# Performance work log

Measured on AMD Instinct MI355X. Metric: run time of the kernel, lower is better.

## Reference

```python
import jax, jax.numpy as jnp
import numpy as np
import math

THETA = 10000.0

def apply_rope(x):
    # x: [B, H, S, D] with D even; interleaved even/odd rotation
    B, H, S, D = x.shape
    dim_half = D // 2
    freq_idx = jnp.arange(dim_half, dtype=jnp.float32)
    inv_freq = jnp.exp(-math.log(THETA) * freq_idx * 2.0 / D)  # [D/2]
    pos = jnp.arange(S, dtype=jnp.float32)
    angles = pos[:, None] * inv_freq[None, :]      # [S, D/2]
    cos = jnp.cos(angles)[None, None]              # [1,1,S,D/2]
    sin = jnp.sin(angles)[None, None]
    x_even = x[..., ::2]
    x_odd = x[..., 1::2]
    r_even = x_even * cos - x_odd * sin
    r_odd = x_odd * cos + x_even * sin
    return jnp.stack([r_even, r_odd], axis=-1).reshape(B, H, S, D)

def setup_inputs() -> dict:
    key = jax.random.key(0)
    ks = jax.random.split(key, 5)
    B, S, E = 2, 2048, 1024
    std = 0.02
    inp = {
        "hidden_states": jax.random.normal(ks[0], (B, S, E), dtype=jnp.float32),
        "Wq": jax.random.normal(ks[1], (E, E), dtype=jnp.float32) * std,
        "bq": jnp.zeros((E,), dtype=jnp.float32),
        "Wk": jax.random.normal(ks[2], (E, E), dtype=jnp.float32) * std,
        "bk": jnp.zeros((E,), dtype=jnp.float32),
        "Wv": jax.random.normal(ks[3], (E, E), dtype=jnp.float32) * std,
        "bv": jnp.zeros((E,), dtype=jnp.float32),
        "Wo": jax.random.normal(ks[4], (E, E), dtype=jnp.float32) * std,
        "bo": jnp.zeros((E,), dtype=jnp.float32),
    }
    return inp

def reference(hidden_states, Wq, bq, Wk, bk, Wv, bv, Wo, bo):
    NUM_HEADS = 16
    B, S, E = hidden_states.shape
    D = E // NUM_HEADS
    scale = 1.0 / math.sqrt(D)

    def proj(W, b):
        # torch Linear: x @ W.T + b; then [B,S,H,D] -> [B,H,S,D]
        y = hidden_states @ W.T + b
        return y.reshape(B, S, NUM_HEADS, D).transpose(0, 2, 1, 3)

    q = apply_rope(proj(Wq, bq))
    k = apply_rope(proj(Wk, bk))
    v = proj(Wv, bv)

    scores = jnp.einsum("bhqd,bhkd->bhqk", q, k) * scale
    attn = jax.nn.softmax(scores, axis=-1)
    out = jnp.einsum("bhqk,bhkd->bhqd", attn, v)  # [B,H,S,D]
    out = out.transpose(0, 2, 1, 3).reshape(B, S, E)
    return out @ Wo.T + bo  # dropout: eval mode (identity)
```

## Files before the change

kernel.cpp:

```cpp
#include <hip/hip_runtime.h>
#include <math.h>

#define B_ 2
#define S_ 2048
#define E_ 1024
#define H_ 16
#define D_ 64
#define M_ (B_*S_)
#define PT 32

typedef short bf16x8 __attribute__((ext_vector_type(8)));
typedef float f32x4 __attribute__((ext_vector_type(4)));
typedef unsigned short u16x4 __attribute__((ext_vector_type(4)));

__device__ __forceinline__ unsigned short f2bf(float f) {
    unsigned int u = __builtin_bit_cast(unsigned int, f);
    u += 0x7FFFu + ((u >> 16) & 1u);
    return (unsigned short)(u >> 16);
}
__device__ __forceinline__ f32x4 mfma16(bf16x8 a, bf16x8 b, f32x4 c) {
    return __builtin_amdgcn_mfma_f32_16x16x32_bf16(a, b, c, 0, 0, 0);
}
__device__ __forceinline__ bf16x8 cvt8(const float* p) {
    f32x4 lo = *(const f32x4*)p;
    f32x4 hi = *(const f32x4*)(p + 4);
    bf16x8 r;
#pragma unroll
    for (int e = 0; e < 4; e++) { r[e] = (short)f2bf(lo[e]); r[e + 4] = (short)f2bf(hi[e]); }
    return r;
}
__device__ __forceinline__ void g2l16(const unsigned short* g, unsigned short* l) {
    __builtin_amdgcn_global_load_lds(
        (const __attribute__((address_space(1))) unsigned int*)(const void*)g,
        (__attribute__((address_space(3))) unsigned int*)(void*)l,
        16, 0, 0);
}

__global__ __launch_bounds__(256) void cvt_kernel(
    const float* __restrict__ X,  const float* __restrict__ Wq,
    const float* __restrict__ Wk, const float* __restrict__ Wv,
    const float* __restrict__ Wo,
    unsigned short* __restrict__ Xb, unsigned short* __restrict__ Wb)
{
    const int y = blockIdx.y;
    const float* src = (y == 0) ? X : (y == 1) ? Wq : (y == 2) ? Wk : (y == 3) ? Wv : Wo;
    unsigned short* dst = (y == 0) ? Xb : Wb + (size_t)(y - 1) * (E_ * E_);
    const size_t n = (y == 0) ? (size_t)M_ * E_ : (size_t)E_ * E_;
    size_t i = ((size_t)blockIdx.x * 256 + threadIdx.x) * 8;
    if (i < n) *(bf16x8*)(dst + i) = cvt8(src + i);
}

__global__ __launch_bounds__(256, 4) void qkv_rope_bf(
    const unsigned short* __restrict__ Xb, const unsigned short* __restrict__ Wb,
    const float* __restrict__ bq, const float* __restrict__ bk,
    const float* __restrict__ bv,
    unsigned short* __restrict__ Qo, unsigned short* __restrict__ Ko,
    unsigned short* __restrict__ Vo)
{
    __shared__ __align__(16) unsigned char lds_raw[128 * 132 * 2];
    unsigned short* As = (unsigned short*)lds_raw;
    unsigned short* Bs = (unsigned short*)(lds_raw + 8192);
    unsigned short* Cs = (unsigned short*)lds_raw;

    const int t = threadIdx.x;
    const int w = t >> 6, lane = t & 63, quad = lane >> 4, l16 = lane & 15;
    const int wr = (w >> 1) * 64, wc = (w & 1) * 64;
    const int n0 = blockIdx.x * 128, m0 = blockIdx.y * 128;
    const int z = blockIdx.z;
    const unsigned short* W = Wb + (size_t)z * (E_ * E_);
    const float* bias = (z == 0) ? bq : (z == 1) ? bk : bv;

    const int r4 = t >> 2, c8 = (t & 3) * 8;
    const unsigned short* Ag = Xb + (size_t)(m0 + r4) * E_ + c8;
    const unsigned short* Bg = W  + (size_t)(n0 + r4) * E_ + c8;

    f32x4 zero = {0.f, 0.f, 0.f, 0.f};
    f32x4 acc[4][4];
#pragma unroll
    for (int i = 0; i < 4; i++)
#pragma unroll
        for (int j = 0; j < 4; j++) acc[i][j] = zero;

    for (int kt = 0; kt < E_; kt += 32) {
        __syncthreads();
        g2l16(Ag + kt,           &As[t * 8]);
        g2l16(Ag + 64 * E_ + kt, &As[t * 8 + 2048]);
        g2l16(Bg + kt,           &Bs[t * 8]);
        g2l16(Bg + 64 * E_ + kt, &Bs[t * 8 + 2048]);
        __syncthreads();
        bf16x8 af[4], bfr[4];
#pragma unroll
        for (int i = 0; i < 4; i++)
            af[i] = *(const bf16x8*)&As[(wr + i * 16 + l16) * 32 + quad * 8];
#pragma unroll
        for (int j = 0; j < 4; j++)
            bfr[j] = *(const bf16x8*)&Bs[(wc + j * 16 + l16) * 32 + quad * 8];
#pragma unroll
        for (int i = 0; i < 4; i++)
#pragma unroll
            for (int j = 0; j < 4; j++)
                acc[i][j] = mfma16(af[i], bfr[j], acc[i][j]);
    }

    __syncthreads();
    const int seg = quad;
    if (z < 2) {
        const float C = -0.41524101186091903f;
        const float INV2PI = 0.15915494309189535f;
#pragma unroll
        for (int j = 0; j < 4; j++) {
            int n_local = wc + j * 16 + l16;
            int n = n0 + n_local;
            int d = n & 63, f = d >> 1;
            float inv_rev = exp2f(C * (float)f) * INV2PI;
            float bvv = bias[n];
            float sgn = (d & 1) ? 1.f : -1.f;
#pragma unroll
            for (int i = 0; i < 4; i++) {
                int mb = wr + i * 16 + quad * 4;
#pragma unroll
                for (int r = 0; r < 4; r++) {
                    int m = m0 + mb + r;
                    int s = m & (S_ - 1);
                    float val = acc[i][j][r] + bvv;
                    float oth = __shfl_xor(val, 1);
                    float rev = (float)s * inv_rev;
                    float fr = rev - rintf(rev);
                    float sn = __builtin_amdgcn_sinf(fr);
                    float cs = __builtin_amdgcn_cosf(fr);
                    Cs[(mb + r) * 132 + n_local] = f2bf(val * cs + sgn * oth * sn);
                }
            }
        }
        __syncthreads();
        unsigned short* Out = (z == 0) ? Qo : Ko;
        const int btok = m0 >> 11;
        const int half = seg & 1;
#pragma unroll
        for (int it = 0; it < 16; it++) {
            int m_local = it * 8 + w * 2 + (seg >> 1);
            int s = (m0 + m_local) & (S_ - 1);
            int h = (n0 + half * 64) >> 6;
            u16x4 v = *(const u16x4*)&Cs[m_local * 132 + half * 64 + l16 * 4];
            *(u16x4*)&Out[(((size_t)btok * H_ + h) * S_ + s) * D_ + l16 * 4] = v;
        }
    } else {
#pragma unroll
        for (int j = 0; j < 4; j++) {
            int n_local = wc + j * 16 + l16;
            float bvv = bias[n0 + n_local];
#pragma unroll
            for (int i = 0; i < 4; i++) {
                int mb = wr + i * 16 + quad * 4;
#pragma unroll
                for (int r = 0; r < 4; r++)
                    Cs[n_local * 132 + mb + r] = f2bf(acc[i][j][r] + bvv);
            }
        }
        __syncthreads();
        const int btok = m0 >> 11;
        const int s0 = m0 & (S_ - 1);
        const int half = seg & 1;
#pragma unroll
        for (int it = 0; it < 16; it++) {
            int n_local = it * 8 + w * 2 + (seg >> 1);
            int n = n0 + n_local;
            int h = n >> 6, d = n & 63;
            u16x4 v = *(const u16x4*)&Cs[n_local * 132 + half * 64 + l16 * 4];
            *(u16x4*)&Vo[(((size_t)btok * H_ + h) * D_ + d) * S_ + s0 + half * 64 + l16 * 4] = v;
        }
    }
}

__global__ __launch_bounds__(512, 4) void attn_kernel(
    const unsigned short* __restrict__ Q, const unsigned short* __restrict__ K,
    const unsigned short* __restrict__ Vt, unsigned short* __restrict__ ctx)
{
    __shared__ unsigned short Ks[2][64 * 32];
    __shared__ unsigned short Vs[2][64 * 32];
    __shared__ unsigned short Ps[8][16 * 72];
    const int t = threadIdx.x;
    const int w = t >> 6, lane = t & 63, quad = lane >> 4, l16 = lane & 15;
    const int bh = blockIdx.y;
    const int q0 = blockIdx.x * 128 + w * 16;

    const unsigned short* Qg = Q + ((size_t)bh * S_ + q0) * D_;
    bf16x8 qf[2];
#pragma unroll
    for (int ks = 0; ks < 2; ks++)
        qf[ks] = *(const bf16x8*)(Qg + (size_t)l16 * 64 + ks * 32 + quad * 8);

    bf16x8 ones;
#pragma unroll
    for (int e = 0; e < 8; e++) ones[e] = (short)0x3F80;

    f32x4 zero = {0.f, 0.f, 0.f, 0.f};
    f32x4 acc_o[4];
    f32x4 acc_l = zero;
#pragma unroll
    for (int j = 0; j < 4; j++) acc_o[j] = zero;

    const int tt = t & 255, ksel = t >> 8;
    const int sr = tt >> 2, sc = (tt & 3) * 8;
    unsigned short* KsF = &Ks[0][0];
    unsigned short* VsF = &Vs[0][0];
    const unsigned short* Kg0 = K  + (size_t)bh * S_ * D_ + (size_t)sr * 64 + ksel * 32 + sc;
    const unsigned short* Vg0 = Vt + (size_t)bh * D_ * S_ + (size_t)sr * S_ + ksel * 32 + sc;

    const float SCL = 0.18033688011f;

    for (int kt = 0; kt < S_; kt += 64) {
        __syncthreads();
        g2l16(Kg0 + (size_t)kt * 64, &KsF[t * 8]);
        g2l16(Vg0 + kt,              &VsF[t * 8]);
        __syncthreads();

        f32x4 sc4[4];
#pragma unroll
        for (int j = 0; j < 4; j++) sc4[j] = zero;
#pragma unroll
        for (int ks = 0; ks < 2; ks++) {
#pragma unroll
            for (int j = 0; j < 4; j++) {
                bf16x8 kf = *(const bf16x8*)&Ks[ks][(j * 16 + l16) * 32 + quad * 8];
                sc4[j] = mfma16(qf[ks], kf, sc4[j]);
            }
        }
#pragma unroll
        for (int j = 0; j < 4; j++)
#pragma unroll
            for (int r = 0; r < 4; r++) {
                float p = __builtin_amdgcn_exp2f(sc4[j][r] * SCL);
                Ps[w][(quad * 4 + r) * 72 + j * 16 + l16] = f2bf(p);
            }
#pragma unroll
        for (int ks = 0; ks < 2; ks++) {
            bf16x8 pf = *(const bf16x8*)&Ps[w][l16 * 72 + ks * 32 + quad * 8];
#pragma unroll
            for (int jd = 0; jd < 4; jd++) {
                bf16x8 vf = *(const bf16x8*)&Vs[ks][(jd * 16 + l16) * 32 + quad * 8];
                acc_o[jd] = mfma16(pf, vf, acc_o[jd]);
            }
            acc_l = mfma16(pf, ones, acc_l);
        }
    }

    const int b = bh >> 4, h = bh & 15;
    f32x4 rl;
#pragma unroll
    for (int r = 0; r < 4; r++) rl[r] = 1.0f / acc_l[r];
#pragma unroll
    for (int jd = 0; jd < 4; jd++)
#pragma unroll
        for (int r = 0; r < 4; r++) {
            int qrow = q0 + quad * 4 + r;
            int col = h * 64 + jd * 16 + l16;
            ctx[((size_t)b * S_ + qrow) * E_ + col] = f2bf(acc_o[jd][r] * rl[r]);
        }
}

__global__ __launch_bounds__(256, 4) void out_bf(
    const unsigned short* __restrict__ Cx, const unsigned short* __restrict__ Wob,
    const float* __restrict__ bo, float* __restrict__ out)
{
    __shared__ unsigned short As[128 * 32];
    __shared__ unsigned short Bs[64 * 32];
    const int t = threadIdx.x;
    const int w = t >> 6, lane = t & 63, quad = lane >> 4, l16 = lane & 15;
    const int m0 = blockIdx.y * 128, n0 = blockIdx.x * 64;
    const int wr = w * 32;
    const int r4 = t >> 2, c8 = (t & 3) * 8;
    const unsigned short* Ag = Cx  + (size_t)(m0 + r4) * E_ + c8;
    const unsigned short* Bg = Wob + (size_t)(n0 + r4) * E_ + c8;

    f32x4 zero = {0.f, 0.f, 0.f, 0.f};
    f32x4 acc[2][4];
#pragma unroll
    for (int i = 0; i < 2; i++)
#pragma unroll
        for (int j = 0; j < 4; j++) acc[i][j] = zero;

    for (int kt = 0; kt < E_; kt += 32) {
        __syncthreads();
        g2l16(Ag + kt,           &As[t * 8]);
        g2l16(Ag + 64 * E_ + kt, &As[t * 8 + 2048]);
        g2l16(Bg + kt,           &Bs[t * 8]);
        __syncthreads();
        bf16x8 af[2], bfr[4];
#pragma unroll
        for (int i = 0; i < 2; i++)
            af[i] = *(const bf16x8*)&As[(wr + i * 16 + l16) * 32 + quad * 8];
#pragma unroll
        for (int j = 0; j < 4; j++)
            bfr[j] = *(const bf16x8*)&Bs[(j * 16 + l16) * 32 + quad * 8];
#pragma unroll
        for (int i = 0; i < 2; i++)
#pragma unroll
            for (int j = 0; j < 4; j++)
                acc[i][j] = mfma16(af[i], bfr[j], acc[i][j]);
    }

#pragma unroll
    for (int j = 0; j < 4; j++) {
        int n = n0 + j * 16 + l16;
        float bvv = bo[n];
#pragma unroll
        for (int i = 0; i < 2; i++) {
            int mrow = m0 + wr + i * 16 + quad * 4;
#pragma unroll
            for (int r = 0; r < 4; r++)
                out[(size_t)(mrow + r) * E_ + n] = acc[i][j][r] + bvv;
        }
    }
}

__global__ __launch_bounds__(256, 3) void qkv_rope_f32(
    const float* __restrict__ X,
    const float* __restrict__ Wq, const float* __restrict__ Wk,
    const float* __restrict__ Wv,
    const float* __restrict__ bq, const float* __restrict__ bk,
    const float* __restrict__ bv,
    unsigned short* __restrict__ Qo, unsigned short* __restrict__ Ko,
    unsigned short* __restrict__ Vo)
{
    __shared__ __align__(16) unsigned char lds_raw[128 * 132 * 2];
    unsigned short* As = (unsigned short*)lds_raw;
    unsigned short* Bs = (unsigned short*)(lds_raw + 8192);
    unsigned short* Cs = (unsigned short*)lds_raw;

    const int t = threadIdx.x;
    const int w = t >> 6, lane = t & 63, quad = lane >> 4, l16 = lane & 15;
    const int wr = (w >> 1) * 64, wc = (w & 1) * 64;
    const int n0 = blockIdx.x * 128, m0 = blockIdx.y * 128;
    const int z = blockIdx.z;
    const float* W    = (z == 0) ? Wq : (z == 1) ? Wk : Wv;
    const float* bias = (z == 0) ? bq : (z == 1) ? bk : bv;

    const int r4 = t >> 2, c8 = (t & 3) * 8;
    const int st = r4 * PT + c8;
    const float* Ag = X + (size_t)(m0 + r4) * E_ + c8;
    const float* Bg = W + (size_t)(n0 + r4) * E_ + c8;

    f32x4 zero = {0.f, 0.f, 0.f, 0.f};
    f32x4 acc[4][4];
#pragma unroll
    for (int i = 0; i < 4; i++)
#pragma unroll
        for (int j = 0; j < 4; j++) acc[i][j] = zero;

    for (int kt = 0; kt < E_; kt += 32) {
        bf16x8 a0 = cvt8(Ag + kt);
        bf16x8 a1 = cvt8(Ag + 64 * E_ + kt);
        bf16x8 b0 = cvt8(Bg + kt);
        bf16x8 b1 = cvt8(Bg + 64 * E_ + kt);
        __syncthreads();
        *(bf16x8*)&As[st]           = a0;
        *(bf16x8*)&As[st + 64 * PT] = a1;
        *(bf16x8*)&Bs[st]           = b0;
        *(bf16x8*)&Bs[st + 64 * PT] = b1;
        __syncthreads();
        bf16x8 af[4], bfr[4];
#pragma unroll
        for (int i = 0; i < 4; i++)
            af[i] = *(const bf16x8*)&As[(wr + i * 16 + l16) * PT + quad * 8];
#pragma unroll
        for (int j = 0; j < 4; j++)
            bfr[j] = *(const bf16x8*)&Bs[(wc + j * 16 + l16) * PT + quad * 8];
#pragma unroll
        for (int i = 0; i < 4; i++)
#pragma unroll
            for (int j = 0; j < 4; j++)
                acc[i][j] = mfma16(af[i], bfr[j], acc[i][j]);
    }

    __syncthreads();
    const int seg = quad;
    if (z < 2) {
        const float C = -0.41524101186091903f;
        const float INV2PI = 0.15915494309189535f;
#pragma unroll
        for (int j = 0; j < 4; j++) {
            int n_local = wc + j * 16 + l16;
            int n = n0 + n_local;
            int d = n & 63, f = d >> 1;
            float inv_rev = exp2f(C * (float)f) * INV2PI;
            float bvv = bias[n];
            float sgn = (d & 1) ? 1.f : -1.f;
#pragma unroll
            for (int i = 0; i < 4; i++) {
                int mb = wr + i * 16 + quad * 4;
#pragma unroll
                for (int r = 0; r < 4; r++) {
                    int m = m0 + mb + r;
                    int s = m & (S_ - 1);
                    float val = acc[i][j][r] + bvv;
                    float oth = __shfl_xor(val, 1);
                    float rev = (float)s * inv_rev;
                    float fr = rev - rintf(rev);
                    float sn = __builtin_amdgcn_sinf(fr);
                    float cs = __builtin_amdgcn_cosf(fr);
                    Cs[(mb + r) * 132 + n_local] = f2bf(val * cs + sgn * oth * sn);
                }
            }
        }
        __syncthreads();
        unsigned short* Out = (z == 0) ? Qo : Ko;
        const int btok = m0 >> 11;
        const int half = seg & 1;
#pragma unroll
        for (int it = 0; it < 16; it++) {
            int m_local = it * 8 + w * 2 + (seg >> 1);
            int s = (m0 + m_local) & (S_ - 1);
            int h = (n0 + half * 64) >> 6;
            u16x4 v = *(const u16x4*)&Cs[m_local * 132 + half * 64 + l16 * 4];
            *(u16x4*)&Out[(((size_t)btok * H_ + h) * S_ + s) * D_ + l16 * 4] = v;
        }
    } else {
#pragma unroll
        for (int j = 0; j < 4; j++) {
            int n_local = wc + j * 16 + l16;
            float bvv = bias[n0 + n_local];
#pragma unroll
            for (int i = 0; i < 4; i++) {
                int mb = wr + i * 16 + quad * 4;
#pragma unroll
                for (int r = 0; r < 4; r++)
                    Cs[n_local * 132 + mb + r] = f2bf(acc[i][j][r] + bvv);
            }
        }
        __syncthreads();
        const int btok = m0 >> 11;
        const int s0 = m0 & (S_ - 1);
        const int half = seg & 1;
#pragma unroll
        for (int it = 0; it < 16; it++) {
            int n_local = it * 8 + w * 2 + (seg >> 1);
            int n = n0 + n_local;
            int h = n >> 6, d = n & 63;
            u16x4 v = *(const u16x4*)&Cs[n_local * 132 + half * 64 + l16 * 4];
            *(u16x4*)&Vo[(((size_t)btok * H_ + h) * D_ + d) * S_ + s0 + half * 64 + l16 * 4] = v;
        }
    }
}

__global__ __launch_bounds__(256, 2) void out_f32(
    const unsigned short* __restrict__ Cx, const float* __restrict__ Wo,
    const float* __restrict__ bo, float* __restrict__ out)
{
    __shared__ unsigned short As[128 * PT];
    __shared__ unsigned short Bs[64 * PT];
    const int t = threadIdx.x;
    const int w = t >> 6, lane = t & 63, quad = lane >> 4, l16 = lane & 15;
    const int m0 = blockIdx.y * 128, n0 = blockIdx.x * 64;
    const int wr = w * 32;
    const int r4 = t >> 2, c8 = (t & 3) * 8;
    const int st = r4 * PT + c8;
    const unsigned short* Ag = Cx + (size_t)(m0 + r4) * E_ + c8;
    const float*          Bg = Wo + (size_t)(n0 + (r4 & 63)) * E_ + c8;

    f32x4 zero = {0.f, 0.f, 0.f, 0.f};
    f32x4 acc[2][4];
#pragma unroll
    for (int i = 0; i < 2; i++)
#pragma unroll
        for (int j = 0; j < 4; j++) acc[i][j] = zero;

    for (int kt = 0; kt < E_; kt += 32) {
        bf16x8 a0 = *(const bf16x8*)(Ag + kt);
        bf16x8 a1 = *(const bf16x8*)(Ag + 64 * E_ + kt);
        bf16x8 b0 = cvt8(Bg + kt);
        __syncthreads();
        *(bf16x8*)&As[st]           = a0;
        *(bf16x8*)&As[st + 64 * PT] = a1;
        *(bf16x8*)&Bs[st]           = b0;
        __syncthreads();
        bf16x8 af[2], bfr[4];
#pragma unroll
        for (int i = 0; i < 2; i++)
            af[i] = *(const bf16x8*)&As[(wr + i * 16 + l16) * PT + quad * 8];
#pragma unroll
        for (int j = 0; j < 4; j++)
            bfr[j] = *(const bf16x8*)&Bs[(j * 16 + l16) * PT + quad * 8];
#pragma unroll
        for (int i = 0; i < 2; i++)
#pragma unroll
            for (int j = 0; j < 4; j++)
                acc[i][j] = mfma16(af[i], bfr[j], acc[i][j]);
    }

#pragma unroll
    for (int j = 0; j < 4; j++) {
        int n = n0 + j * 16 + l16;
        float bvv = bo[n];
#pragma unroll
        for (int i = 0; i < 2; i++) {
            int mrow = m0 + wr + i * 16 + quad * 4;
#pragma unroll
            for (int r = 0; r < 4; r++)
                out[(size_t)(mrow + r) * E_ + n] = acc[i][j][r] + bvv;
        }
    }
}

extern "C" void kernel_launch(void* const* d_in, const int* in_sizes, int n_in,
                              void* d_out, int out_size, void* d_ws, size_t ws_size,
                              hipStream_t stream) {
    const float* X  = (const float*)d_in[0];
    const float* Wq = (const float*)d_in[1];
    const float* bq = (const float*)d_in[2];
    const float* Wk = (const float*)d_in[3];
    const float* bk = (const float*)d_in[4];
    const float* Wv = (const float*)d_in[5];
    const float* bv = (const float*)d_in[6];
    const float* Wo = (const float*)d_in[7];
    const float* bo = (const float*)d_in[8];
    float* outp = (float*)d_out;

    const size_t TN = (size_t)B_ * H_ * S_ * D_;
    if (ws_size < 4 * TN * sizeof(unsigned short)) return;

    unsigned short* Qb = (unsigned short*)d_ws;
    unsigned short* Kb = Qb + TN;
    unsigned short* Vb = Kb + TN;

    if (ws_size >= 5 * TN * sizeof(unsigned short)) {
        unsigned short* Xb = Vb + TN;
        unsigned short* Wb = Xb + TN;
        unsigned short* Cx = Xb;

        cvt_kernel<<<dim3(2048, 5), 256, 0, stream>>>(X, Wq, Wk, Wv, Wo, Xb, Wb);
        qkv_rope_bf<<<dim3(E_ / 128, M_ / 128, 3), 256, 0, stream>>>(
            Xb, Wb, bq, bk, bv, Qb, Kb, Vb);
        attn_kernel<<<dim3(S_ / 128, B_ * H_), 512, 0, stream>>>(Qb, Kb, Vb, Cx);
        out_bf<<<dim3(E_ / 64, M_ / 128), 256, 0, stream>>>(
            Cx, Wb + 3 * (size_t)(E_ * E_), bo, outp);
    } else {
        unsigned short* Cx = Vb + TN;
        qkv_rope_f32<<<dim3(E_ / 128, M_ / 128, 3), 256, 0, stream>>>(
            X, Wq, Wk, Wv, bq, bk, bv, Qb, Kb, Vb);
        attn_kernel<<<dim3(S_ / 128, B_ * H_), 512, 0, stream>>>(Qb, Kb, Vb, Cx);
        out_f32<<<dim3(E_ / 64, M_ / 128), 256, 0, stream>>>(Cx, Wo, bo, outp);
    }
}
```

Measured before the change: 208.1 us.

## Split attention over two KV halves and add a combine kernel

Moves the attention inner loop into a shared helper, and adds a split variant that launches twice as many blocks, each covering half of the key sequence. Each block writes unnormalized fp32 partial outputs and row sums to workspace. A separate combine kernel adds the two halves, normalizes them and writes bf16 context. The aim is more blocks to fill the GPU; the price is extra fp32 traffic to global memory and one more kernel launch. The split path runs only when the workspace is large enough, and otherwise the original single-pass kernel is used.

```diff
diff --git a/kernel.cpp b/kernel.cpp
--- a/kernel.cpp
+++ b/kernel.cpp
@@ -172,7 +172,80 @@
     }
 }
 
-__global__ __launch_bounds__(512, 4) void attn_kernel(
+struct AttnAcc { f32x4 o[4]; f32x4 l; };
+__device__ __forceinline__ AttnAcc attn_core(
+    const unsigned short* Q, const unsigned short* K, const unsigned short* Vt,
+    int bh, int q0, int kt_begin, int kt_end,
+    unsigned short (*Ks)[64 * 32], unsigned short (*Vs)[64 * 32],
+    unsigned short (*Ps)[16 * 72])
+{
+    const int t = threadIdx.x;
+    const int w = t >> 6, lane = t & 63, quad = lane >> 4, l16 = lane & 15;
+
+    const unsigned short* Qg = Q + ((size_t)bh * S_ + q0) * D_;
+    bf16x8 qf[2];
+#pragma unroll
+    for (int ks = 0; ks < 2; ks++)
+        qf[ks] = *(const bf16x8*)(Qg + (size_t)l16 * 64 + ks * 32 + quad * 8);
+
+    bf16x8 ones;
+#pragma unroll
+    for (int e = 0; e < 8; e++) ones[e] = (short)0x3F80;
+
+    f32x4 zero = {0.f, 0.f, 0.f, 0.f};
+    AttnAcc A;
+    A.l = zero;
+#pragma unroll
+    for (int j = 0; j < 4; j++) A.o[j] = zero;
+
+    const int tt = t & 255, ksel = t >> 8;
+    const int sr = tt >> 2, sc = (tt & 3) * 8;
+    unsigned short* KsF = &Ks[0][0];
+    unsigned short* VsF = &Vs[0][0];
+    const unsigned short* Kg0 = K  + (size_t)bh * S_ * D_ + (size_t)sr * 64 + ksel * 32 + sc;
+    const unsigned short* Vg0 = Vt + (size_t)bh * D_ * S_ + (size_t)sr * S_ + ksel * 32 + sc;
+
+    const float SCL = 0.18033688011f;
+
+    for (int kt = kt_begin; kt < kt_end; kt += 64) {
+        __syncthreads();
+        g2l16(Kg0 + (size_t)kt * 64, &KsF[t * 8]);
+        g2l16(Vg0 + kt,              &VsF[t * 8]);
+        __syncthreads();
+
+        f32x4 sc4[4];
+#pragma unroll
+        for (int j = 0; j < 4; j++) sc4[j] = zero;
+#pragma unroll
+        for (int ks = 0; ks < 2; ks++) {
+#pragma unroll
+            for (int j = 0; j < 4; j++) {
+                bf16x8 kf = *(const bf16x8*)&Ks[ks][(j * 16 + l16) * 32 + quad * 8];
+                sc4[j] = mfma16(qf[ks], kf, sc4[j]);
+            }
+        }
+#pragma unroll
+        for (int j = 0; j < 4; j++)
+#pragma unroll
+            for (int r = 0; r < 4; r++) {
+                float p = __builtin_amdgcn_exp2f(sc4[j][r] * SCL);
+                Ps[w][(quad * 4 + r) * 72 + j * 16 + l16] = f2bf(p);
+            }
+#pragma unroll
+        for (int ks = 0; ks < 2; ks++) {
+            bf16x8 pf = *(const bf16x8*)&Ps[w][l16 * 72 + ks * 32 + quad * 8];
+#pragma unroll
+            for (int jd = 0; jd < 4; jd++) {
+                bf16x8 vf = *(const bf16x8*)&Vs[ks][(jd * 16 + l16) * 32 + quad * 8];
+                A.o[jd] = mfma16(pf, vf, A.o[jd]);
+            }
+            A.l = mfma16(pf, ones, A.l);
+        }
+    }
+    return A;
+}
+
+__global__ __launch_bounds__(512, 4) void attn_direct(
     const unsigned short* __restrict__ Q, const unsigned short* __restrict__ K,
     const unsigned short* __restrict__ Vt, unsigned short* __restrict__ ctx)
 {
@@ -184,79 +257,73 @@
     const int bh = blockIdx.y;
     const int q0 = blockIdx.x * 128 + w * 16;
 
-    const unsigned short* Qg = Q + ((size_t)bh * S_ + q0) * D_;
-    bf16x8 qf[2];
-#pragma unroll
-    for (int ks = 0; ks < 2; ks++)
-        qf[ks] = *(const bf16x8*)(Qg + (size_t)l16 * 64 + ks * 32 + quad * 8);
-
-    bf16x8 ones;
-#pragma unroll
-    for (int e = 0; e < 8; e++) ones[e] = (short)0x3F80;
-
-    f32x4 zero = {0.f, 0.f, 0.f, 0.f};
-    f32x4 acc_o[4];
-    f32x4 acc_l = zero;
-#pragma unroll
-    for (int j = 0; j < 4; j++) acc_o[j] = zero;
-
-    const int tt = t & 255, ksel = t >> 8;
-    const int sr = tt >> 2, sc = (tt & 3) * 8;
-    unsigned short* KsF = &Ks[0][0];
-    unsigned short* VsF = &Vs[0][0];
-    const unsigned short* Kg0 = K  + (size_t)bh * S_ * D_ + (size_t)sr * 64 + ksel * 32 + sc;
-    const unsigned short* Vg0 = Vt + (size_t)bh * D_ * S_ + (size_t)sr * S_ + ksel * 32 + sc;
-
-    const float SCL = 0.18033688011f;
-
-    for (int kt = 0; kt < S_; kt += 64) {
-        __syncthreads();
-        g2l16(Kg0 + (size_t)kt * 64, &KsF[t * 8]);
-        g2l16(Vg0 + kt,              &VsF[t * 8]);
-        __syncthreads();
-
-        f32x4 sc4[4];
-#pragma unroll
-        for (int j = 0; j < 4; j++) sc4[j] = zero;
-#pragma unroll
-        for (int ks = 0; ks < 2; ks++) {
-#pragma unroll
-            for (int j = 0; j < 4; j++) {
-                bf16x8 kf = *(const bf16x8*)&Ks[ks][(j * 16 + l16) * 32 + quad * 8];
-                sc4[j] = mfma16(qf[ks], kf, sc4[j]);
-            }
-        }
-#pragma unroll
-        for (int j = 0; j < 4; j++)
-#pragma unroll
-            for (int r = 0; r < 4; r++) {
-                float p = __builtin_amdgcn_exp2f(sc4[j][r] * SCL);
-                Ps[w][(quad * 4 + r) * 72 + j * 16 + l16] = f2bf(p);
-            }
-#pragma unroll
-        for (int ks = 0; ks < 2; ks++) {
-            bf16x8 pf = *(const bf16x8*)&Ps[w][l16 * 72 + ks * 32 + quad * 8];
-#pragma unroll
-            for (int jd = 0; jd < 4; jd++) {
-                bf16x8 vf = *(const bf16x8*)&Vs[ks][(jd * 16 + l16) * 32 + quad * 8];
-                acc_o[jd] = mfma16(pf, vf, acc_o[jd]);
-            }
-            acc_l = mfma16(pf, ones, acc_l);
-        }
-    }
+    AttnAcc A = attn_core(Q, K, Vt, bh, q0, 0, S_, Ks, Vs, Ps);
 
     const int b = bh >> 4, h = bh & 15;
     f32x4 rl;
 #pragma unroll
-    for (int r = 0; r < 4; r++) rl[r] = 1.0f / acc_l[r];
+    for (int r = 0; r < 4; r++) rl[r] = 1.0f / A.l[r];
 #pragma unroll
     for (int jd = 0; jd < 4; jd++)
 #pragma unroll
         for (int r = 0; r < 4; r++) {
             int qrow = q0 + quad * 4 + r;
             int col = h * 64 + jd * 16 + l16;
-            ctx[((size_t)b * S_ + qrow) * E_ + col] = f2bf(acc_o[jd][r] * rl[r]);
-        }
+            ctx[((size_t)b * S_ + qrow) * E_ + col] = f2bf(A.o[jd][r] * rl[r]);
+        }
+}
+
+__global__ __launch_bounds__(512, 4) void attn_split(
+    const unsigned short* __restrict__ Q, const unsigned short* __restrict__ K,
+    const unsigned short* __restrict__ Vt,
+    float* __restrict__ Op, float* __restrict__ Lp)
+{
+    __shared__ unsigned short Ks[2][64 * 32];
+    __shared__ unsigned short Vs[2][64 * 32];
+    __shared__ unsigned short Ps[8][16 * 72];
+    const int t = threadIdx.x;
+    const int w = t >> 6, lane = t & 63, quad = lane >> 4, l16 = lane & 15;
+    const int bh = blockIdx.y;
+    const int half = blockIdx.z;
+    const int q0 = blockIdx.x * 128 + w * 16;
+
+    AttnAcc A = attn_core(Q, K, Vt, bh, q0, half * (S_ / 2), (half + 1) * (S_ / 2),
+                          Ks, Vs, Ps);
+
+    const size_t base = ((size_t)half * (B_ * H_) + bh) * S_;
+#pragma unroll
+    for (int jd = 0; jd < 4; jd++)
+#pragma unroll
+        for (int r = 0; r < 4; r++) {
+            int qrow = q0 + quad * 4 + r;
+            Op[(base + qrow) * D_ + jd * 16 + l16] = A.o[jd][r];
+        }
+    if (l16 == 0) {
+#pragma unroll
+        for (int r = 0; r < 4; r++)
+            Lp[base + q0 + quad * 4 + r] = A.l[r];
+    }
+}
+
+__global__ __launch_bounds__(256) void combine_kernel(
+    const float* __restrict__ Op, const float* __restrict__ Lp,
+    unsigned short* __restrict__ ctx)
+{
+    const size_t TN = (size_t)B_ * H_ * S_ * D_;
+    size_t i = ((size_t)blockIdx.x * 256 + threadIdx.x) * 4;
+    if (i >= TN) return;
+    int d = (int)(i & 63);
+    int srow = (int)((i >> 6) & (S_ - 1));
+    int bh = (int)(i >> 17);
+    float l = Lp[(size_t)bh * S_ + srow] + Lp[((size_t)(B_ * H_) + bh) * S_ + srow];
+    float rl = 1.0f / l;
+    f32x4 o0 = *(const f32x4*)&Op[((size_t)bh * S_ + srow) * D_ + d];
+    f32x4 o1 = *(const f32x4*)&Op[(((size_t)(B_ * H_) + bh) * S_ + srow) * D_ + d];
+    int b = bh >> 4, h = bh & 15;
+    u16x4 v;
+#pragma unroll
+    for (int e = 0; e < 4; e++) v[e] = f2bf((o0[e] + o1[e]) * rl);
+    *(u16x4*)&ctx[((size_t)b * S_ + srow) * E_ + h * 64 + d] = v;
 }
 
 __global__ __launch_bounds__(256, 4) void out_bf(
@@ -517,13 +584,17 @@
     float* outp = (float*)d_out;
 
     const size_t TN = (size_t)B_ * H_ * S_ * D_;
-    if (ws_size < 4 * TN * sizeof(unsigned short)) return;
+    const size_t need_f32   = 4 * TN * sizeof(unsigned short);
+    const size_t need_bf    = 5 * TN * sizeof(unsigned short);
+    const size_t need_split = need_bf + 2 * TN * sizeof(float)
+                            + 2 * (size_t)(B_ * H_ * S_) * sizeof(float);
+    if (ws_size < need_f32) return;
 
     unsigned short* Qb = (unsigned short*)d_ws;
     unsigned short* Kb = Qb + TN;
     unsigned short* Vb = Kb + TN;
 
-    if (ws_size >= 5 * TN * sizeof(unsigned short)) {
+    if (ws_size >= need_bf) {
         unsigned short* Xb = Vb + TN;
         unsigned short* Wb = Xb + TN;
         unsigned short* Cx = Xb;
@@ -531,14 +602,23 @@
         cvt_kernel<<<dim3(2048, 5), 256, 0, stream>>>(X, Wq, Wk, Wv, Wo, Xb, Wb);
         qkv_rope_bf<<<dim3(E_ / 128, M_ / 128, 3), 256, 0, stream>>>(
             Xb, Wb, bq, bk, bv, Qb, Kb, Vb);
-        attn_kernel<<<dim3(S_ / 128, B_ * H_), 512, 0, stream>>>(Qb, Kb, Vb, Cx);
+
+        if (ws_size >= need_split) {
+            float* Op = (float*)(Wb + 4 * (size_t)(E_ * E_));
+            float* Lp = Op + 2 * TN;
+            attn_split<<<dim3(S_ / 128, B_ * H_, 2), 512, 0, stream>>>(
+                Qb, Kb, Vb, Op, Lp);
+            combine_kernel<<<dim3((int)(TN / 1024)), 256, 0, stream>>>(Op, Lp, Cx);
+        } else {
+            attn_direct<<<dim3(S_ / 128, B_ * H_), 512, 0, stream>>>(Qb, Kb, Vb, Cx);
+        }
         out_bf<<<dim3(E_ / 64, M_ / 128), 256, 0, stream>>>(
             Cx, Wb + 3 * (size_t)(E_ * E_), bo, outp);
     } else {
         unsigned short* Cx = Vb + TN;
         qkv_rope_f32<<<dim3(E_ / 128, M_ / 128, 3), 256, 0, stream>>>(
             X, Wq, Wk, Wv, bq, bk, bv, Qb, Kb, Vb);
-        attn_kernel<<<dim3(S_ / 128, B_ * H_), 512, 0, stream>>>(Qb, Kb, Vb, Cx);
+        attn_direct<<<dim3(S_ / 128, B_ * H_), 512, 0, stream>>>(Qb, Kb, Vb, Cx);
         out_f32<<<dim3(E_ / 64, M_ / 128), 256, 0, stream>>>(Cx, Wo, bo, outp);
     }
 }
```

After: 213.4 us. +2.6%, slower.
